# Kernel optimization log

Hardware: AMD Instinct MI355X
Metric: run time of the kernel (lower is better)

The kernel has to match this reference:

```python
import jax, jax.numpy as jnp
import numpy as np

N, C, HD = 8192, 1024, 128

def setup_inputs() -> dict:
    key = jax.random.key(0)
    ks = jax.random.split(key, 9)
    def xavier(k, fan_in, fan_out):
        lim = float(np.sqrt(6.0 / (fan_in + fan_out)))
        return jax.random.uniform(k, (fan_out, fan_in), jnp.float32, -lim, lim)
    return {
        "x": jax.random.normal(ks[0], (N, C), jnp.float32),
        "Wq": xavier(ks[1], C, HD), "bq": jnp.zeros((HD,), jnp.float32),
        "Wk": xavier(ks[2], C, HD), "bk": jnp.zeros((HD,), jnp.float32),
        "Wv": xavier(ks[3], C, C),  "bv": jnp.zeros((C,), jnp.float32),
        "Wo": xavier(ks[4], C, C),  "bo": jnp.zeros((C,), jnp.float32),
    }

def reference(x, Wq, bq, Wk, bk, Wv, bv, Wo, bo):
    scale = HD ** -0.5
    q = x @ Wq.T + bq          # (N, HD)
    k = x @ Wk.T + bk          # (N, HD)
    v = x @ Wv.T + bv          # (N, C)
    scores = (q @ k.T) * scale # (N, N)
    attn = jax.nn.softmax(scores, axis=-1)
    out = attn @ v             # (N, C)
    return out @ Wo.T + bo
```

## Files before the change

kernel.cpp:

```cpp
#include <hip/hip_runtime.h>

#define NTOK 8192
#define CDIM 1024
#define HDIM 128

typedef __attribute__((ext_vector_type(8))) short short8;
typedef __attribute__((ext_vector_type(4))) float floatx4;
typedef __attribute__((ext_vector_type(4))) unsigned short ushort4v;

__device__ inline unsigned short f2bf(float f) {
    union { float f; unsigned u; } v; v.f = f;
    unsigned r = v.u + 0x7fffu + ((v.u >> 16) & 1u);
    return (unsigned short)(r >> 16);
}
__device__ inline unsigned short f2bf_fast(float f) {
    union { float f; unsigned u; } v; v.f = f;
    return (unsigned short)((v.u + 0x8000u) >> 16);
}
__device__ inline float bf2f(short s) {
    union { unsigned u; float f; } v;
    v.u = ((unsigned)(unsigned short)s) << 16;
    return v.f;
}
__device__ inline void async16(const unsigned short* g, short* l) {
    __builtin_amdgcn_global_load_lds(
        (const __attribute__((address_space(1))) unsigned*)g,
        (__attribute__((address_space(3))) unsigned*)l, 16, 0, 0);
}

__global__ void cast_f32_bf16(const float* __restrict__ in,
                              unsigned short* __restrict__ out, int n4) {
    int i = blockIdx.x * blockDim.x + threadIdx.x;
    if (i < n4) {
        float4 v = ((const float4*)in)[i];
        ushort4 o;
        o.x = f2bf(v.x); o.y = f2bf(v.y); o.z = f2bf(v.z); o.w = f2bf(v.w);
        ((ushort4*)out)[i] = o;
    }
}

template<int SWZ>
__global__ __launch_bounds__(256) void gemm_nt(
    const unsigned short* __restrict__ A, const unsigned short* __restrict__ W,
    const float* __restrict__ bias, unsigned short* __restrict__ out, int M, int N, int K)
{
    __shared__ short As[4][64][8];
    __shared__ short Ws[4][64][8];
    const int tid = threadIdx.x;
    const int wave = tid >> 6, lane = tid & 63;
    const int lr = lane & 15, lc = lane >> 4;
    const int m0 = blockIdx.x * 64, n0 = blockIdx.y * 64;

    floatx4 acc[4] = {};
    const int srow = tid >> 2, sch = tid & 3;
    const unsigned short* Ag = A + (long)(m0 + srow) * K + sch * 8;
    const unsigned short* Wg = W + (long)(n0 + srow) * K + sch * 8;

    for (int k0 = 0; k0 < K; k0 += 32) {
        *(short8*)&As[sch][srow][0] = *(const short8*)(Ag + k0);
        *(short8*)&Ws[sch][srow][0] = *(const short8*)(Wg + k0);
        __syncthreads();
        short8 a = *(short8*)&As[lc][wave * 16 + lr][0];
#pragma unroll
        for (int s = 0; s < 4; s++) {
            short8 b = *(short8*)&Ws[lc][s * 16 + lr][0];
            acc[s] = __builtin_amdgcn_mfma_f32_16x16x32_bf16(a, b, acc[s], 0, 0, 0);
        }
        __syncthreads();
    }

#pragma unroll
    for (int s = 0; s < 4; s++) {
        int h = n0 + s * 16 + lr;
        float bv = bias[h];
        int tok0 = m0 + wave * 16 + lc * 4;
#pragma unroll
        for (int r = 0; r < 4; r++) {
            int tok = tok0 + r;
            if (SWZ)
                out[(tok >> 5) * 4096 + (h >> 3) * 256 + (tok & 31) * 8 + (h & 7)] =
                    f2bf(acc[s][r] + bv);
            else
                out[(long)tok * N + h] = f2bf(acc[s][r] + bv);
        }
    }
}

template<int MODE>
__global__ __launch_bounds__(256) void gemm128_nt(
    const unsigned short* __restrict__ A, const unsigned short* __restrict__ W,
    const float* __restrict__ bias, void* __restrict__ out, int M, int N, int K)
{
    __shared__ short As[128][4][8];
    __shared__ short Ws[128][4][8];
    const int tid = threadIdx.x, wave = tid >> 6, lane = tid & 63;
    const int lr = lane & 15, lc = lane >> 4;
    const int wm = (wave >> 1) * 64, wn = (wave & 1) * 64;
    const int m0 = blockIdx.x * 128, n0 = blockIdx.y * 128;

    floatx4 acc[4][4] = {};

    const int srow = lane >> 2, sch = lane & 3;
    const unsigned short* Ag0 = A + (long)(m0 + wave * 32 + srow) * K + sch * 8;
    const unsigned short* Ag1 = Ag0 + (long)16 * K;
    const unsigned short* Wg0 = W + (long)(n0 + wave * 32 + srow) * K + sch * 8;
    const unsigned short* Wg1 = Wg0 + (long)16 * K;
    short* lA0 = &As[wave * 32][0][0];
    short* lA1 = &As[wave * 32 + 16][0][0];
    short* lW0 = &Ws[wave * 32][0][0];
    short* lW1 = &Ws[wave * 32 + 16][0][0];

    for (int k0 = 0; k0 < K; k0 += 32) {
        async16(Ag0 + k0, lA0);
        async16(Ag1 + k0, lA1);
        async16(Wg0 + k0, lW0);
        async16(Wg1 + k0, lW1);
        __syncthreads();
        short8 af[4], bfg[4];
#pragma unroll
        for (int i = 0; i < 4; i++) af[i]  = *(short8*)&As[wm + i * 16 + lr][lc][0];
#pragma unroll
        for (int j = 0; j < 4; j++) bfg[j] = *(short8*)&Ws[wn + j * 16 + lr][lc][0];
#pragma unroll
        for (int i = 0; i < 4; i++)
#pragma unroll
            for (int j = 0; j < 4; j++)
                acc[i][j] = __builtin_amdgcn_mfma_f32_16x16x32_bf16(af[i], bfg[j], acc[i][j], 0, 0, 0);
        __syncthreads();
    }

#pragma unroll
    for (int i = 0; i < 4; i++) {
        int t0 = m0 + wm + i * 16 + lc * 4;
#pragma unroll
        for (int j = 0; j < 4; j++) {
            int c = n0 + wn + j * 16 + lr;
            float bv = bias[c];
            if (MODE == 0) {
                float* o = (float*)out;
#pragma unroll
                for (int r = 0; r < 4; r++) o[(long)(t0 + r) * N + c] = acc[i][j][r] + bv;
            } else {
                unsigned short* o = (unsigned short*)out;
                ushort4 pk;
                pk.x = f2bf(acc[i][j][0] + bv); pk.y = f2bf(acc[i][j][1] + bv);
                pk.z = f2bf(acc[i][j][2] + bv); pk.w = f2bf(acc[i][j][3] + bv);
                long off = (long)(c >> 8) * 2097152 + (t0 >> 5) * 8192 +
                           ((t0 & 31) >> 3) * 2048 + (c & 255) * 8 + (t0 & 7);
                *(ushort4*)&o[off] = pk;
            }
        }
    }
}

__global__ __launch_bounds__(256, 2) void attn_pv(
    const unsigned short* __restrict__ qb, const unsigned short* __restrict__ ksw,
    const unsigned short* __restrict__ vsw,
    unsigned short* __restrict__ Oa, unsigned short* __restrict__ Ob,
    float* __restrict__ la, float* __restrict__ lb)
{
    __shared__ short Ks[2][16][32][8];
    __shared__ short Vs[2][4][256][8];
    __shared__ short Ps[4][32][40];

    const int tid = threadIdx.x, wave = tid >> 6, lane = tid & 63;
    const int lr = lane & 15, lc = lane >> 4;
    const int m0 = blockIdx.x * 128, cblk = blockIdx.y;
    const int mw = m0 + wave * 32;
    const int nt0 = blockIdx.z * 128;
    unsigned short* Op = blockIdx.z ? Ob : Oa;
    float* ls = blockIdx.z ? lb : la;
    const float cexp = (float)(0.08838834764831845 * 1.4426950408889634);

    short8 qf[2][4];
#pragma unroll
    for (int ms = 0; ms < 2; ms++)
#pragma unroll
        for (int kk = 0; kk < 4; kk++)
            qf[ms][kk] = *(const short8*)&qb[(mw + ms * 16 + lr) * HDIM + kk * 32 + lc * 8];

    floatx4 acc[2][16] = {};
    float lsum[2] = {};

    const unsigned short* kg[2];
    short* const klb = &Ks[0][0][0][0];
#pragma unroll
    for (int t = 0; t < 2; t++) kg[t] = ksw + (wave * 2 + t) * 512 + lane * 8;
    const unsigned short* vg[4];
    short* const vlb = &Vs[0][0][0][0];
#pragma unroll
    for (int t = 0; t < 4; t++)
        vg[t] = vsw + (long)cblk * 2097152 + (wave * 4 + t) * 512 + lane * 8;

    {
        long nt = nt0;
#pragma unroll
        for (int t = 0; t < 2; t++)
            async16(kg[t] + nt * 4096, klb + (wave * 2 + t) * 512);
#pragma unroll
        for (int t = 0; t < 4; t++)
            async16(vg[t] + nt * 8192, vlb + (wave * 4 + t) * 512);
    }

    for (int it = 0; it < 128; ++it) {
        const int buf = it & 1;
        __syncthreads();
        if (it + 1 < 128) {
            long nt = nt0 + it + 1;
#pragma unroll
            for (int t = 0; t < 2; t++)
                async16(kg[t] + nt * 4096, klb + (buf ^ 1) * 4096 + (wave * 2 + t) * 512);
#pragma unroll
            for (int t = 0; t < 4; t++)
                async16(vg[t] + nt * 8192,
                        vlb + (buf ^ 1) * 8192 + (wave * 4 + t) * 512);
        }

        floatx4 st[2][2] = {};
#pragma unroll
        for (int kk = 0; kk < 4; kk++) {
            short8 kf0 = *(short8*)&Ks[buf][kk * 4 + lc][lr][0];
            short8 kf1 = *(short8*)&Ks[buf][kk * 4 + lc][16 + lr][0];
#pragma unroll
            for (int ms = 0; ms < 2; ms++) {
                st[ms][0] = __builtin_amdgcn_mfma_f32_16x16x32_bf16(kf0, qf[ms][kk], st[ms][0], 0, 0, 0);
                st[ms][1] = __builtin_amdgcn_mfma_f32_16x16x32_bf16(kf1, qf[ms][kk], st[ms][1], 0, 0, 0);
            }
        }
#pragma unroll
        for (int ms = 0; ms < 2; ms++)
#pragma unroll
            for (int sub = 0; sub < 2; sub++) {
                ushort4v pk;
#pragma unroll
                for (int r = 0; r < 4; r++) {
                    float p = __builtin_amdgcn_exp2f(st[ms][sub][r] * cexp);
                    lsum[ms] += p;
                    pk[r] = f2bf_fast(p);
                }
                *(ushort4v*)&Ps[wave][ms * 16 + lr][sub * 16 + lc * 4] = pk;
            }
        short8 ap[2];
#pragma unroll
        for (int ms = 0; ms < 2; ms++) ap[ms] = *(short8*)&Ps[wave][ms * 16 + lr][lc * 8];
#pragma unroll
        for (int csh = 0; csh < 2; csh++) {
            short8 bv[8];
#pragma unroll
            for (int cs = 0; cs < 8; cs++)
                bv[cs] = *(short8*)&Vs[buf][lc][(csh * 8 + cs) * 16 + lr][0];
#pragma unroll
            for (int ms = 0; ms < 2; ms++)
#pragma unroll
                for (int cs = 0; cs < 8; cs++)
                    acc[ms][csh * 8 + cs] =
                        __builtin_amdgcn_mfma_f32_16x16x32_bf16(ap[ms], bv[cs], acc[ms][csh * 8 + cs], 0, 0, 0);
        }
    }

#pragma unroll
    for (int ms = 0; ms < 2; ms++)
#pragma unroll
        for (int cs = 0; cs < 16; cs++) {
            int c = cblk * 256 + cs * 16 + lr;
#pragma unroll
            for (int r = 0; r < 4; r++)
                Op[(long)(mw + ms * 16 + lc * 4 + r) * CDIM + c] = f2bf(acc[ms][cs][r]);
        }
    if (blockIdx.y == 0) {
#pragma unroll
        for (int ms = 0; ms < 2; ms++) {
            lsum[ms] += __shfl_xor(lsum[ms], 16);
            lsum[ms] += __shfl_xor(lsum[ms], 32);
        }
        if (lc == 0) {
#pragma unroll
            for (int ms = 0; ms < 2; ms++) ls[mw + ms * 16 + lr] = lsum[ms];
        }
    }
}

__global__ __launch_bounds__(256) void combine_attn(
    const unsigned short* __restrict__ Oa, unsigned short* __restrict__ Ob,
    const float* __restrict__ la, const float* __restrict__ lb)
{
    int i = blockIdx.x * blockDim.x + threadIdx.x;
    int row = i >> 7;
    float inv = 1.0f / (la[row] + lb[row]);
    short8 a = ((const short8*)Oa)[i];
    short8 b = ((const short8*)Ob)[i];
    short8 o;
#pragma unroll
    for (int e = 0; e < 8; e++) o[e] = (short)f2bf((bf2f(a[e]) + bf2f(b[e])) * inv);
    ((short8*)Ob)[i] = o;
}

extern "C" void kernel_launch(void* const* d_in, const int* in_sizes, int n_in,
                              void* d_out, int out_size, void* d_ws, size_t ws_size,
                              hipStream_t stream) {
    const float* x  = (const float*)d_in[0];
    const float* Wq = (const float*)d_in[1];
    const float* bq = (const float*)d_in[2];
    const float* Wk = (const float*)d_in[3];
    const float* bk = (const float*)d_in[4];
    const float* Wv = (const float*)d_in[5];
    const float* bv = (const float*)d_in[6];
    const float* Wo = (const float*)d_in[7];
    const float* bo = (const float*)d_in[8];

    char* ws = (char*)d_ws;
    unsigned short* x_bf   = (unsigned short*)(ws + 0);
    unsigned short* wq_bf  = (unsigned short*)(ws + 16777216);
    unsigned short* wk_bf  = (unsigned short*)(ws + 17039360);
    unsigned short* wv_bf  = (unsigned short*)(ws + 17301504);
    unsigned short* wo_bf  = (unsigned short*)(ws + 19398656);
    unsigned short* q_bf   = (unsigned short*)(ws + 21495808);
    unsigned short* k_swz  = (unsigned short*)(ws + 23592960);
    unsigned short* v_swz  = (unsigned short*)(ws + 25690112);
    unsigned short* attn_bf= (unsigned short*)(ws + 42467328);
    float* lsum_a          = (float*)(ws + 59244544);
    float* lsum_b          = (float*)(ws + 59277312);

    cast_f32_bf16<<<8192, 256, 0, stream>>>(x,  x_bf,  2097152);
    cast_f32_bf16<<<128,  256, 0, stream>>>(Wq, wq_bf, 32768);
    cast_f32_bf16<<<128,  256, 0, stream>>>(Wk, wk_bf, 32768);
    cast_f32_bf16<<<1024, 256, 0, stream>>>(Wv, wv_bf, 262144);
    cast_f32_bf16<<<1024, 256, 0, stream>>>(Wo, wo_bf, 262144);

    gemm_nt<0><<<dim3(128, 2), 256, 0, stream>>>(x_bf, wq_bf, bq, q_bf, NTOK, HDIM, CDIM);
    gemm_nt<1><<<dim3(128, 2), 256, 0, stream>>>(x_bf, wk_bf, bk, k_swz, NTOK, HDIM, CDIM);
    gemm128_nt<2><<<dim3(64, 8), 256, 0, stream>>>(x_bf, wv_bf, bv, v_swz, NTOK, CDIM, CDIM);

    attn_pv<<<dim3(64, 4, 2), 256, 0, stream>>>(q_bf, k_swz, v_swz,
                                                x_bf, attn_bf, lsum_a, lsum_b);
    combine_attn<<<4096, 256, 0, stream>>>(x_bf, attn_bf, lsum_a, lsum_b);

    gemm128_nt<0><<<dim3(64, 8), 256, 0, stream>>>(attn_bf, wo_bf, bo, d_out, NTOK, CDIM, CDIM);
}
```

Measured before the change: 400.7 us.

## Software-pipeline PV MFMA one iteration behind QK and softmax

Restructures the attention loop so the P·V accumulation for iteration it-1 runs before the QK scores and exp for iteration it, with a drain step after the loop. V gets a triple-buffered LDS ring with rotating read, middle and write pointers. The aim is to interleave the PV MFMA chain with the score computation and hide the latency of the P round-trip through LDS. It uses more LDS, which may cut occupancy, and Ps is written and read by the same wave across iterations with no extra barrier.

New measurement: 396.5 us. No clear change (-1.0%).

```diff
diff --git a/kernel.cpp b/kernel.cpp
--- a/kernel.cpp
+++ b/kernel.cpp
@@ -160,7 +160,7 @@
     float* __restrict__ la, float* __restrict__ lb)
 {
     __shared__ short Ks[2][16][32][8];
-    __shared__ short Vs[2][4][256][8];
+    __shared__ short Vs[3][4][256][8];
     __shared__ short Ps[4][32][40];
 
     const int tid = threadIdx.x, wave = tid >> 6, lane = tid & 63;
@@ -187,11 +187,14 @@
 #pragma unroll
     for (int t = 0; t < 2; t++) kg[t] = ksw + (wave * 2 + t) * 512 + lane * 8;
     const unsigned short* vg[4];
-    short* const vlb = &Vs[0][0][0][0];
 #pragma unroll
     for (int t = 0; t < 4; t++)
         vg[t] = vsw + (long)cblk * 2097152 + (wave * 4 + t) * 512 + lane * 8;
 
+    short* v_r = &Vs[2][0][0][0];
+    short* v_m = &Vs[0][0][0][0];
+    short* v_w = &Vs[1][0][0][0];
+
     {
         long nt = nt0;
 #pragma unroll
@@ -199,7 +202,7 @@
             async16(kg[t] + nt * 4096, klb + (wave * 2 + t) * 512);
 #pragma unroll
         for (int t = 0; t < 4; t++)
-            async16(vg[t] + nt * 8192, vlb + (wave * 4 + t) * 512);
+            async16(vg[t] + nt * 8192, v_m + (wave * 4 + t) * 512);
     }
 
     for (int it = 0; it < 128; ++it) {
@@ -212,8 +215,26 @@
                 async16(kg[t] + nt * 4096, klb + (buf ^ 1) * 4096 + (wave * 2 + t) * 512);
 #pragma unroll
             for (int t = 0; t < 4; t++)
-                async16(vg[t] + nt * 8192,
-                        vlb + (buf ^ 1) * 8192 + (wave * 4 + t) * 512);
+                async16(vg[t] + nt * 8192, v_w + (wave * 4 + t) * 512);
+        }
+
+        if (it > 0) {
+            short8 ap[2];
+#pragma unroll
+            for (int ms = 0; ms < 2; ms++) ap[ms] = *(short8*)&Ps[wave][ms * 16 + lr][lc * 8];
+#pragma unroll
+            for (int csh = 0; csh < 2; csh++) {
+                short8 bv[8];
+#pragma unroll
+                for (int cs = 0; cs < 8; cs++)
+                    bv[cs] = *(short8*)(v_r + lc * 2048 + ((csh * 8 + cs) * 16 + lr) * 8);
+#pragma unroll
+                for (int ms = 0; ms < 2; ms++)
+#pragma unroll
+                    for (int cs = 0; cs < 8; cs++)
+                        acc[ms][csh * 8 + cs] =
+                            __builtin_amdgcn_mfma_f32_16x16x32_bf16(ap[ms], bv[cs], acc[ms][csh * 8 + cs], 0, 0, 0);
+            }
         }
 
         floatx4 st[2][2] = {};
@@ -227,6 +248,7 @@
                 st[ms][1] = __builtin_amdgcn_mfma_f32_16x16x32_bf16(kf1, qf[ms][kk], st[ms][1], 0, 0, 0);
             }
         }
+
 #pragma unroll
         for (int ms = 0; ms < 2; ms++)
 #pragma unroll
@@ -240,6 +262,11 @@
                 }
                 *(ushort4v*)&Ps[wave][ms * 16 + lr][sub * 16 + lc * 4] = pk;
             }
+
+        short* tmp = v_r; v_r = v_m; v_m = v_w; v_w = tmp;
+    }
+
+    {
         short8 ap[2];
 #pragma unroll
         for (int ms = 0; ms < 2; ms++) ap[ms] = *(short8*)&Ps[wave][ms * 16 + lr][lc * 8];
@@ -248,7 +275,7 @@
             short8 bv[8];
 #pragma unroll
             for (int cs = 0; cs < 8; cs++)
-                bv[cs] = *(short8*)&Vs[buf][lc][(csh * 8 + cs) * 16 + lr][0];
+                bv[cs] = *(short8*)(v_r + lc * 2048 + ((csh * 8 + cs) * 16 + lr) * 8);
 #pragma unroll
             for (int ms = 0; ms < 2; ms++)
 #pragma unroll
```
